# Kernel tuning notes

Measured on AMD Instinct MI355X. Metric: run time of the kernel, lower is better.

## Reference

```python
import jax, jax.numpy as jnp
import numpy as np

N = 203769
E = 234355
IN, HID, OUT = 165, 128, 64
EPS = 1e-5


def setup_inputs() -> dict:
    key = jax.random.key(0)
    ks = jax.random.split(key, 12)
    x = jax.random.normal(ks[0], (N, IN), dtype=jnp.float32)
    edge_index = jax.random.randint(ks[1], (2, E), 0, N, dtype=jnp.int64)
    s = lambda fan: 1.0 / np.sqrt(fan)
    W1 = jax.random.uniform(ks[2], (IN, HID), jnp.float32, -s(IN), s(IN))
    b1 = jnp.zeros((HID,), jnp.float32)
    g1 = jnp.ones((HID,), jnp.float32)
    be1 = jnp.zeros((HID,), jnp.float32)
    W2 = jax.random.uniform(ks[3], (HID, OUT), jnp.float32, -s(HID), s(HID))
    b2 = jnp.zeros((OUT,), jnp.float32)
    g2 = jnp.ones((OUT,), jnp.float32)
    be2 = jnp.zeros((OUT,), jnp.float32)
    Wp1 = jax.random.uniform(ks[4], (OUT, OUT), jnp.float32, -s(OUT), s(OUT))
    bp1 = jax.random.uniform(ks[5], (OUT,), jnp.float32, -s(OUT), s(OUT))
    Wp2 = jax.random.uniform(ks[6], (OUT, OUT), jnp.float32, -s(OUT), s(OUT))
    bp2 = jax.random.uniform(ks[7], (OUT,), jnp.float32, -s(OUT), s(OUT))
    return {"x": x, "edge_index": edge_index, "W1": W1, "b1": b1, "g1": g1, "be1": be1,
            "W2": W2, "b2": b2, "g2": g2, "be2": be2,
            "Wp1": Wp1, "bp1": bp1, "Wp2": Wp2, "bp2": bp2}


def gcn_conv(x, W, b, src, dst, n):
    # PyG GCNConv: h = xW; add self-loops; sym-normalized aggregation; + bias
    h = x @ W  # [N, F]
    loop = jnp.arange(n, dtype=src.dtype)
    s = jnp.concatenate([src, loop])
    d = jnp.concatenate([dst, loop])
    w = jnp.ones(s.shape[0], x.dtype)  # edge_weight=None -> ones
    deg = jax.ops.segment_sum(w, d, num_segments=n)
    dinv = jnp.where(deg > 0, jax.lax.rsqrt(deg), 0.0)
    norm = dinv[s] * w * dinv[d]  # [E+N]
    msg = h[s] * norm[:, None]    # gather + scale
    return jax.ops.segment_sum(msg, d, num_segments=n) + b


def batch_norm(x, g, be):
    m = jnp.mean(x, axis=0)
    v = jnp.mean(jnp.square(x - m), axis=0)  # biased var (torch BN)
    return (x - m) * jax.lax.rsqrt(v + EPS) * g + be


def reference(x, edge_index, W1, b1, g1, be1, W2, b2, g2, be2, Wp1, bp1, Wp2, bp2):
    src, dst = edge_index[0], edge_index[1]
    n = x.shape[0]
    h = gcn_conv(x, W1, b1, src, dst, n)
    h = jax.nn.relu(batch_norm(h, g1, be1))  # dropout omitted (eval / deterministic)
    h = gcn_conv(h, W2, b2, src, dst, n)
    h = batch_norm(h, g2, be2)  # last layer: no relu/dropout
    z = jax.nn.relu(h @ Wp1 + bp1) @ Wp2 + bp2
    return (h, z)
```

## Files before the change

kernel.cpp:

```cpp
#include <hip/hip_runtime.h>
#include <hip/hip_bf16.h>

#define N_NODES 203769
#define N_EDGES 234355
#define F_IN    165
#define F_HID   128
#define F_OUT   64
#define BN_EPS  1e-5f
#define NB_SCAN 796
#define KP      192
#define NBLK    1024
#define GB128C  1593
#define RGP     (GB128C * 8)

typedef short bf16x8 __attribute__((ext_vector_type(8)));
typedef unsigned short u16x8 __attribute__((ext_vector_type(8)));
typedef float f32x4 __attribute__((ext_vector_type(4)));

__device__ __forceinline__ unsigned short f2bf(float f) {
    unsigned int u = __builtin_bit_cast(unsigned int, f);
    u += 0x7fffu + ((u >> 16) & 1u);
    return (unsigned short)(u >> 16);
}

__global__ void k_count(const int* __restrict__ dst, int* __restrict__ cnt) {
    int e = blockIdx.x * 256 + threadIdx.x;
    if (e < N_EDGES) atomicAdd(&cnt[dst[e]], 1);
}

__global__ __launch_bounds__(256) void k_scanA(const int* __restrict__ cnt,
                                               int* __restrict__ partials) {
    __shared__ int sm[256];
    int t = threadIdx.x;
    int i = blockIdx.x * 256 + t;
    int v = (i < N_NODES) ? cnt[i] : 0;
    sm[t] = v;
    __syncthreads();
    for (int off = 128; off > 0; off >>= 1) {
        if (t < off) sm[t] += sm[t + off];
        __syncthreads();
    }
    if (t == 0) partials[blockIdx.x] = sm[0];
}

__global__ __launch_bounds__(1024) void k_scanB(int* __restrict__ partials,
                                                int* __restrict__ row_ptr) {
    __shared__ int sm[1024];
    int t = threadIdx.x;
    int v = (t < NB_SCAN) ? partials[t] : 0;
    sm[t] = v;
    __syncthreads();
    for (int off = 1; off < 1024; off <<= 1) {
        int add = (t >= off) ? sm[t - off] : 0;
        __syncthreads();
        sm[t] += add;
        __syncthreads();
    }
    if (t < NB_SCAN) partials[t] = sm[t] - v;
    if (t == NB_SCAN - 1) row_ptr[N_NODES] = sm[t];
}

__global__ __launch_bounds__(256) void k_scanC(const int* __restrict__ cnt,
                                               const int* __restrict__ partials,
                                               int* __restrict__ row_ptr,
                                               int* __restrict__ cursor,
                                               float* __restrict__ dinv) {
    __shared__ int sm[256];
    int t = threadIdx.x;
    int i = blockIdx.x * 256 + t;
    int v = (i < N_NODES) ? cnt[i] : 0;
    sm[t] = v;
    __syncthreads();
    for (int off = 1; off < 256; off <<= 1) {
        int add = (t >= off) ? sm[t - off] : 0;
        __syncthreads();
        sm[t] += add;
        __syncthreads();
    }
    if (i < N_NODES) {
        int p = partials[blockIdx.x] + sm[t] - v;
        row_ptr[i] = p;
        cursor[i] = p;
        dinv[i] = rsqrtf(1.0f + (float)v);
    }
}

__global__ void k_scatter(const int* __restrict__ src, const int* __restrict__ dst,
                          int* __restrict__ cursor, int* __restrict__ csr_src) {
    int e = blockIdx.x * 256 + threadIdx.x;
    if (e < N_EDGES) {
        int pos = atomicAdd(&cursor[dst[e]], 1);
        csr_src[pos] = src[e];
    }
}

__global__ void k_cvt_w(const float* __restrict__ W1, unsigned short* __restrict__ wb) {
    int i = blockIdx.x * 256 + threadIdx.x;
    if (i < F_HID * KP) {
        int n = i / KP, k = i - n * KP;
        float v = (k < F_IN) ? W1[k * F_HID + n] : 0.0f;
        int ng = n >> 4, l16 = n & 15, kb = k >> 5, quad = (k >> 3) & 3, j = k & 7;
        wb[((((size_t)ng * 6 + kb) * 4 + quad) * 16 + l16) * 8 + j] = f2bf(v);
    }
}

__global__ __launch_bounds__(256) void k_cvt_x(const float* __restrict__ x,
                                               unsigned short* __restrict__ xa) {
    __shared__ unsigned short xt[16 * 200];
    const int rg = blockIdx.x;
    const int t = threadIdx.x;
    const int row0 = rg * 16;

    if (row0 + 16 <= N_NODES) {
        const float* slab = x + (size_t)row0 * F_IN;
        for (int u = t; u < 660; u += 256) {
            float4 v = *(const float4*)&slab[u * 4];
            float vv[4] = {v.x, v.y, v.z, v.w};
            int f0 = u * 4;
#pragma unroll
            for (int j = 0; j < 4; j++) {
                int f = f0 + j;
                int r = f / 165;
                int k = f - r * 165;
                xt[r * 200 + k] = f2bf(vv[j]);
            }
        }
    } else {
        for (int u = t; u < 660; u += 256) {
            int f0 = u * 4;
#pragma unroll
            for (int j = 0; j < 4; j++) {
                int f = f0 + j;
                int r = f / 165;
                int k = f - r * 165;
                int row = row0 + r;
                float val = (row < N_NODES) ? x[(size_t)row * F_IN + k] : 0.0f;
                xt[r * 200 + k] = f2bf(val);
            }
        }
    }
    __syncthreads();

    for (int v = t; v < 384; v += 256) {
        int l16 = v & 15;
        int quad = (v >> 4) & 3;
        int kb = v >> 6;
        int k0 = kb * 32 + quad * 8;
        u16x8 uv;
#pragma unroll
        for (int j = 0; j < 8; j++) {
            int k = k0 + j;
            uv[j] = (k < F_IN) ? xt[l16 * 200 + k] : (unsigned short)0;
        }
        *(u16x8*)&xa[((size_t)rg * 384 + v) * 8] = uv;
    }
}

__global__ __launch_bounds__(256) void k_mfma1(const unsigned short* __restrict__ xa,
                                               const unsigned short* __restrict__ wb,
                                               const float* __restrict__ dinv,
                                               float* __restrict__ h1s) {
    const int t = threadIdx.x;
    const int wv = t >> 6;
    const int lane = t & 63;
    const int l16 = lane & 15;
    const int quad = lane >> 4;
    const int rg0 = blockIdx.x * 8 + wv * 2;
    const int lq = quad * 16 + l16;

    f32x4 acc[2][8];
#pragma unroll
    for (int mt = 0; mt < 2; mt++)
#pragma unroll
        for (int nt = 0; nt < 8; nt++)
            acc[mt][nt] = (f32x4){0.0f, 0.0f, 0.0f, 0.0f};

#pragma unroll
    for (int kb = 0; kb < 6; kb++) {
        bf16x8 a[2], b[8];
#pragma unroll
        for (int mt = 0; mt < 2; mt++)
            a[mt] = *(const bf16x8*)&xa[(((size_t)(rg0 + mt) * 6 + kb) * 64 + lq) * 8];
#pragma unroll
        for (int nt = 0; nt < 8; nt++)
            b[nt] = *(const bf16x8*)&wb[(((size_t)nt * 6 + kb) * 64 + lq) * 8];
#pragma unroll
        for (int mt = 0; mt < 2; mt++)
#pragma unroll
            for (int nt = 0; nt < 8; nt++)
                acc[mt][nt] = __builtin_amdgcn_mfma_f32_16x16x32_bf16(
                    a[mt], b[nt], acc[mt][nt], 0, 0, 0);
    }

#pragma unroll
    for (int mt = 0; mt < 2; mt++) {
#pragma unroll
        for (int rgi = 0; rgi < 4; rgi++) {
            int grow = (rg0 + mt) * 16 + quad * 4 + rgi;
            if (grow < N_NODES) {
                float dv = dinv[grow];
                float* orow = h1s + (size_t)grow * F_HID + l16;
#pragma unroll
                for (int nt = 0; nt < 8; nt++)
                    orow[nt * 16] = acc[mt][nt][rgi] * dv;
            }
        }
    }
}

template <int C, int TPN, int NPB>
__global__ __launch_bounds__(256) void k_aggr(const float* __restrict__ hs,
                                              const int* __restrict__ row_ptr,
                                              const int* __restrict__ csr_src,
                                              const float* __restrict__ dinv,
                                              float* __restrict__ out,
                                              float* __restrict__ psum,
                                              float* __restrict__ psq) {
    const int t = threadIdx.x;
    const int q = t & (TPN - 1);
    const int slot = t / TPN;
    float s0 = 0, s1 = 0, s2 = 0, s3 = 0;
    float q0 = 0, q1 = 0, q2 = 0, q3 = 0;

    for (int node = blockIdx.x * NPB + slot; node < N_NODES;
         node += gridDim.x * NPB) {
        int beg = row_ptr[node];
        int end = row_ptr[node + 1];
        float4 acc = *(const float4*)&hs[(size_t)node * C + q * 4];
        for (int e = beg; e < end; e++) {
            int s = csr_src[e];
            float4 v = *(const float4*)&hs[(size_t)s * C + q * 4];
            acc.x += v.x; acc.y += v.y; acc.z += v.z; acc.w += v.w;
        }
        float dv = dinv[node];
        acc.x *= dv; acc.y *= dv; acc.z *= dv; acc.w *= dv;
        *(float4*)&out[(size_t)node * C + q * 4] = acc;
        s0 += acc.x; s1 += acc.y; s2 += acc.z; s3 += acc.w;
        q0 = fmaf(acc.x, acc.x, q0); q1 = fmaf(acc.y, acc.y, q1);
        q2 = fmaf(acc.z, acc.z, q2); q3 = fmaf(acc.w, acc.w, q3);
    }

    __shared__ float sm[256 * 4];
    __shared__ float sq[256 * 4];
    sm[t * 4 + 0] = s0; sm[t * 4 + 1] = s1; sm[t * 4 + 2] = s2; sm[t * 4 + 3] = s3;
    sq[t * 4 + 0] = q0; sq[t * 4 + 1] = q1; sq[t * 4 + 2] = q2; sq[t * 4 + 3] = q3;
    __syncthreads();
    if (t < TPN) {
#pragma unroll
        for (int sl = 1; sl < NPB; sl++) {
            int u = (sl * TPN + t) * 4;
            s0 += sm[u + 0]; s1 += sm[u + 1]; s2 += sm[u + 2]; s3 += sm[u + 3];
            q0 += sq[u + 0]; q1 += sq[u + 1]; q2 += sq[u + 2]; q3 += sq[u + 3];
        }
        float4 o1 = {s0, s1, s2, s3};
        float4 o2 = {q0, q1, q2, q3};
        *(float4*)&psum[(size_t)blockIdx.x * C + t * 4] = o1;
        *(float4*)&psq [(size_t)blockIdx.x * C + t * 4] = o2;
    }
}

template <int C>
__global__ __launch_bounds__(1024) void k_bn_fin(const float* __restrict__ psum,
                                                 const float* __restrict__ psq,
                                                 const float* __restrict__ g,
                                                 const float* __restrict__ be,
                                                 float* __restrict__ sc,
                                                 float* __restrict__ sh) {
    const int t = threadIdx.x;
    const int c = t & (C - 1);
    const int gg = t / C;
    const int G = 1024 / C;
    const int BPG = NBLK / G;
    float s = 0.0f, sq_ = 0.0f;
    for (int i = 0; i < BPG; i++) {
        int b = gg * BPG + i;
        s   += psum[(size_t)b * C + c];
        sq_ += psq [(size_t)b * C + c];
    }
    __shared__ float sm[1024];
    __shared__ float s2[1024];
    sm[t] = s;
    s2[t] = sq_;
    __syncthreads();
    for (int off = G / 2; off > 0; off >>= 1) {
        if (gg < off) {
            sm[t] += sm[t + off * C];
            s2[t] += s2[t + off * C];
        }
        __syncthreads();
    }
    if (gg == 0) {
        const float invn = 1.0f / (float)N_NODES;
        float mean = sm[c] * invn;
        float var = s2[c] * invn - mean * mean;
        float rstd = rsqrtf(var + BN_EPS);
        float scale = g[c] * rstd;
        sc[c] = scale;
        sh[c] = fmaf(-mean, scale, be[c]);
    }
}

__global__ __launch_bounds__(256) void k_gemm2(const float* __restrict__ out1,
                                               const float* __restrict__ sc1,
                                               const float* __restrict__ sh1,
                                               const float* __restrict__ W2,
                                               const float* __restrict__ dinv,
                                               float* __restrict__ h2s) {
    __shared__ float xs[64 * 132];
    const int row0 = blockIdx.x * 64;
    const int t = threadIdx.x;
    {
        const float* src = out1 + (size_t)row0 * F_HID;
        const int maxe = (N_NODES - row0) * F_HID;
        for (int fi = t; fi < 64 * F_HID; fi += 256) {
            int r = fi >> 7;
            int c = fi & 127;
            float v = (fi < maxe) ? src[fi] : 0.0f;
            v = fmaf(v, sc1[c], sh1[c]);
            xs[r * 132 + c] = fmaxf(v, 0.0f);
        }
    }
    __syncthreads();

    const int c0 = (t & 15) * 4;
    const int r0 = (t >> 4) * 4;

    float acc[4][4];
#pragma unroll
    for (int r = 0; r < 4; r++)
#pragma unroll
        for (int c = 0; c < 4; c++) acc[r][c] = 0.0f;

#pragma unroll 2
    for (int k4 = 0; k4 < F_HID; k4 += 4) {
        float4 xv[4];
#pragma unroll
        for (int r = 0; r < 4; r++)
            xv[r] = *(const float4*)&xs[(r0 + r) * 132 + k4];
        float4 w[4];
#pragma unroll
        for (int j = 0; j < 4; j++)
            w[j] = *(const float4*)&W2[(k4 + j) * F_OUT + c0];
#pragma unroll
        for (int r = 0; r < 4; r++) {
            const float xr[4] = {xv[r].x, xv[r].y, xv[r].z, xv[r].w};
#pragma unroll
            for (int j = 0; j < 4; j++) {
                acc[r][0] = fmaf(xr[j], w[j].x, acc[r][0]);
                acc[r][1] = fmaf(xr[j], w[j].y, acc[r][1]);
                acc[r][2] = fmaf(xr[j], w[j].z, acc[r][2]);
                acc[r][3] = fmaf(xr[j], w[j].w, acc[r][3]);
            }
        }
    }
#pragma unroll
    for (int r = 0; r < 4; r++) {
        int row = row0 + r0 + r;
        if (row < N_NODES) {
            float dv = dinv[row];
            float4 o = {acc[r][0] * dv, acc[r][1] * dv, acc[r][2] * dv, acc[r][3] * dv};
            *(float4*)&h2s[(size_t)row * F_OUT + c0] = o;
        }
    }
}

__global__ __launch_bounds__(256) void k_final(const float* __restrict__ out2,
                                               const float* __restrict__ sc2,
                                               const float* __restrict__ sh2,
                                               const float* __restrict__ Wp1,
                                               const float* __restrict__ bp1,
                                               const float* __restrict__ Wp2,
                                               const float* __restrict__ bp2,
                                               float* __restrict__ out) {
    __shared__ float hs[64 * 68];
    __shared__ float as_[64 * 68];
    const int row0 = blockIdx.x * 64;
    const int t = threadIdx.x;

    {
        const float4* src = (const float4*)out2;
        float4* dsth = (float4*)out;
#pragma unroll
        for (int i = 0; i < 4; i++) {
            int f4 = t + i * 256;
            int r = f4 >> 4;
            int c4 = f4 & 15;
            int grow = row0 + r;
            float4 v = {0, 0, 0, 0};
            if (grow < N_NODES) v = src[(size_t)grow * 16 + c4];
            int c = c4 * 4;
            v.x = fmaf(v.x, sc2[c + 0], sh2[c + 0]);
            v.y = fmaf(v.y, sc2[c + 1], sh2[c + 1]);
            v.z = fmaf(v.z, sc2[c + 2], sh2[c + 2]);
            v.w = fmaf(v.w, sc2[c + 3], sh2[c + 3]);
            if (grow < N_NODES) dsth[(size_t)grow * 16 + c4] = v;
            *(float4*)&hs[r * 68 + c] = v;
        }
    }
    __syncthreads();

    const int c0 = (t & 15) * 4;
    const int r0 = (t >> 4) * 4;

    {
        float acc[4][4];
#pragma unroll
        for (int r = 0; r < 4; r++)
#pragma unroll
            for (int c = 0; c < 4; c++) acc[r][c] = 0.0f;
#pragma unroll 2
        for (int k4 = 0; k4 < 64; k4 += 4) {
            float4 xv[4];
#pragma unroll
            for (int r = 0; r < 4; r++)
                xv[r] = *(const float4*)&hs[(r0 + r) * 68 + k4];
            float4 w[4];
#pragma unroll
            for (int j = 0; j < 4; j++)
                w[j] = *(const float4*)&Wp1[(k4 + j) * 64 + c0];
#pragma unroll
            for (int r = 0; r < 4; r++) {
                const float xr[4] = {xv[r].x, xv[r].y, xv[r].z, xv[r].w};
#pragma unroll
                for (int j = 0; j < 4; j++) {
                    acc[r][0] = fmaf(xr[j], w[j].x, acc[r][0]);
                    acc[r][1] = fmaf(xr[j], w[j].y, acc[r][1]);
                    acc[r][2] = fmaf(xr[j], w[j].z, acc[r][2]);
                    acc[r][3] = fmaf(xr[j], w[j].w, acc[r][3]);
                }
            }
        }
        float4 b = *(const float4*)&bp1[c0];
#pragma unroll
        for (int r = 0; r < 4; r++) {
            float4 o = {fmaxf(acc[r][0] + b.x, 0.0f), fmaxf(acc[r][1] + b.y, 0.0f),
                        fmaxf(acc[r][2] + b.z, 0.0f), fmaxf(acc[r][3] + b.w, 0.0f)};
            *(float4*)&as_[(r0 + r) * 68 + c0] = o;
        }
    }
    __syncthreads();

    {
        float acc[4][4];
#pragma unroll
        for (int r = 0; r < 4; r++)
#pragma unroll
            for (int c = 0; c < 4; c++) acc[r][c] = 0.0f;
#pragma unroll 2
        for (int k4 = 0; k4 < 64; k4 += 4) {
            float4 xv[4];
#pragma unroll
            for (int r = 0; r < 4; r++)
                xv[r] = *(const float4*)&as_[(r0 + r) * 68 + k4];
            float4 w[4];
#pragma unroll
            for (int j = 0; j < 4; j++)
                w[j] = *(const float4*)&Wp2[(k4 + j) * 64 + c0];
#pragma unroll
            for (int r = 0; r < 4; r++) {
                const float xr[4] = {xv[r].x, xv[r].y, xv[r].z, xv[r].w};
#pragma unroll
                for (int j = 0; j < 4; j++) {
                    acc[r][0] = fmaf(xr[j], w[j].x, acc[r][0]);
                    acc[r][1] = fmaf(xr[j], w[j].y, acc[r][1]);
                    acc[r][2] = fmaf(xr[j], w[j].z, acc[r][2]);
                    acc[r][3] = fmaf(xr[j], w[j].w, acc[r][3]);
                }
            }
        }
        float4 b = *(const float4*)&bp2[c0];
        float* zout = out + (size_t)N_NODES * 64;
#pragma unroll
        for (int r = 0; r < 4; r++) {
            int row = row0 + r0 + r;
            if (row < N_NODES) {
                float4 o = {acc[r][0] + b.x, acc[r][1] + b.y,
                            acc[r][2] + b.z, acc[r][3] + b.w};
                *(float4*)&zout[(size_t)row * 64 + c0] = o;
            }
        }
    }
}

extern "C" void kernel_launch(void* const* d_in, const int* in_sizes, int n_in,
                              void* d_out, int out_size, void* d_ws, size_t ws_size,
                              hipStream_t stream) {
    const float* x   = (const float*)d_in[0];
    const int*   ei  = (const int*)d_in[1];
    const float* W1  = (const float*)d_in[2];
    const float* g1  = (const float*)d_in[4];
    const float* be1 = (const float*)d_in[5];
    const float* W2  = (const float*)d_in[6];
    const float* g2  = (const float*)d_in[8];
    const float* be2 = (const float*)d_in[9];
    const float* Wp1 = (const float*)d_in[10];
    const float* bp1 = (const float*)d_in[11];
    const float* Wp2 = (const float*)d_in[12];
    const float* bp2 = (const float*)d_in[13];

    const int* src = ei;
    const int* dst = ei + N_EDGES;

    float* ws = (float*)d_ws;
    float* A    = ws;
    float* B    = A + (size_t)N_NODES * 128;
    float* dinv = B + (size_t)N_NODES * 128;
    float* st   = dinv + N_NODES;
    float* sc1  = st + 256;  float* sh1  = st + 384;
    float* sc2  = st + 640;  float* sh2  = st + 704;
    int* cnt      = (int*)(st + 768);
    int* row_ptr  = cnt + N_NODES;
    int* cursor   = row_ptr + N_NODES + 1;
    int* csr_src  = cursor + N_NODES;
    int* partials = csr_src + N_EDGES;
    unsigned short* wb = (unsigned short*)(partials + NB_SCAN);

    size_t off = (size_t)((char*)(wb + F_HID * KP) - (char*)d_ws);
    off = (off + 15) & ~(size_t)15;
    float* ps1  = (float*)((char*)d_ws + off);
    float* ps1q = ps1 + (size_t)NBLK * 128;
    float* ps2  = ps1q + (size_t)NBLK * 128;
    float* ps2q = ps2 + (size_t)NBLK * 64;
    unsigned short* xa = (unsigned short*)(ps2q + (size_t)NBLK * 64);

    hipMemsetAsync(st, 0, (768 + N_NODES) * sizeof(float), stream);

    const int EB = (N_EDGES + 255) / 256;
    const int GB64 = (N_NODES + 63) / 64;

    k_count<<<EB, 256, 0, stream>>>(dst, cnt);
    k_cvt_w<<<(F_HID * KP + 255) / 256, 256, 0, stream>>>(W1, wb);
    k_cvt_x<<<RGP, 256, 0, stream>>>(x, xa);
    k_scanA<<<NB_SCAN, 256, 0, stream>>>(cnt, partials);
    k_scanB<<<1, 1024, 0, stream>>>(partials, row_ptr);
    k_scanC<<<NB_SCAN, 256, 0, stream>>>(cnt, partials, row_ptr, cursor, dinv);
    k_scatter<<<EB, 256, 0, stream>>>(src, dst, cursor, csr_src);

    k_mfma1<<<GB128C, 256, 0, stream>>>(xa, wb, dinv, A);
    k_aggr<128, 32, 8><<<NBLK, 256, 0, stream>>>(A, row_ptr, csr_src, dinv, B, ps1, ps1q);
    k_bn_fin<128><<<1, 1024, 0, stream>>>(ps1, ps1q, g1, be1, sc1, sh1);

    k_gemm2<<<GB64, 256, 0, stream>>>(B, sc1, sh1, W2, dinv, A);
    k_aggr<64, 16, 16><<<NBLK, 256, 0, stream>>>(A, row_ptr, csr_src, dinv, B, ps2, ps2q);
    k_bn_fin<64><<<1, 1024, 0, stream>>>(ps2, ps2q, g2, be2, sc2, sh2);

    k_final<<<GB64, 256, 0, stream>>>(B, sc2, sh2, Wp1, bp1, Wp2, bp2, (float*)d_out);
}
```

Before: 601.5 us.

## Replace FP32 layer-2 GEMM with split-bf16 MFMA kernel

Replaces the scalar FP32 shared-memory GEMM for layer 2 with an MFMA kernel. Activations (after BN+ReLU) and W2 are each split into bf16 high and low parts, and three MFMAs per tile (hi*hi, lo*hi, hi*lo) keep near-FP32 accuracy. W2 is pre-split by a new small conversion kernel into an MFMA-friendly layout. The aim is to cut VALU FMA cost and the LDS staging, in exchange for extra conversion arithmetic and a slightly different rounding behaviour.

Measured after the change: 546.7 us. -9.1%, faster.

```diff
diff --git a/kernel.cpp b/kernel.cpp
--- a/kernel.cpp
+++ b/kernel.cpp
@@ -22,6 +22,10 @@
     u += 0x7fffu + ((u >> 16) & 1u);
     return (unsigned short)(u >> 16);
 }
+__device__ __forceinline__ float bf2f(unsigned short h) {
+    unsigned int u = ((unsigned int)h) << 16;
+    return __builtin_bit_cast(float, u);
+}
 
 __global__ void k_count(const int* __restrict__ dst, int* __restrict__ cnt) {
     int e = blockIdx.x * 256 + threadIdx.x;
@@ -101,6 +105,22 @@
         float v = (k < F_IN) ? W1[k * F_HID + n] : 0.0f;
         int ng = n >> 4, l16 = n & 15, kb = k >> 5, quad = (k >> 3) & 3, j = k & 7;
         wb[((((size_t)ng * 6 + kb) * 4 + quad) * 16 + l16) * 8 + j] = f2bf(v);
+    }
+}
+
+__global__ void k_cvt_w2(const float* __restrict__ W2,
+                         unsigned short* __restrict__ w2h,
+                         unsigned short* __restrict__ w2l) {
+    int i = blockIdx.x * 256 + threadIdx.x;
+    if (i < F_HID * F_OUT) {
+        int k = i / F_OUT, n = i - k * F_OUT;
+        float v = W2[i];
+        unsigned short h = f2bf(v);
+        float lo = v - bf2f(h);
+        int ng = n >> 4, l16 = n & 15, kb = k >> 5, quad = (k >> 3) & 3, j = k & 7;
+        size_t idx = ((((size_t)ng * 4 + kb) * 4 + quad) * 16 + l16) * 8 + j;
+        w2h[idx] = h;
+        w2l[idx] = f2bf(lo);
     }
 }
 
@@ -202,6 +222,102 @@
                 float* orow = h1s + (size_t)grow * F_HID + l16;
 #pragma unroll
                 for (int nt = 0; nt < 8; nt++)
+                    orow[nt * 16] = acc[mt][nt][rgi] * dv;
+            }
+        }
+    }
+}
+
+__global__ __launch_bounds__(256) void k_mfma2(const float* __restrict__ out1,
+                                               const float* __restrict__ sc1,
+                                               const float* __restrict__ sh1,
+                                               const unsigned short* __restrict__ w2h,
+                                               const unsigned short* __restrict__ w2l,
+                                               const float* __restrict__ dinv,
+                                               float* __restrict__ h2s) {
+    const int t = threadIdx.x;
+    const int wv = t >> 6;
+    const int lane = t & 63;
+    const int l16 = lane & 15;
+    const int quad = lane >> 4;
+    const int rg0 = blockIdx.x * 8 + wv * 2;
+    const int lq = quad * 16 + l16;
+
+    f32x4 acc[2][4];
+#pragma unroll
+    for (int mt = 0; mt < 2; mt++)
+#pragma unroll
+        for (int nt = 0; nt < 4; nt++)
+            acc[mt][nt] = (f32x4){0.0f, 0.0f, 0.0f, 0.0f};
+
+#pragma unroll
+    for (int kb = 0; kb < 4; kb++) {
+        const int k0 = kb * 32 + quad * 8;
+        float4 sA = *(const float4*)&sc1[k0];
+        float4 sB = *(const float4*)&sc1[k0 + 4];
+        float4 hA = *(const float4*)&sh1[k0];
+        float4 hB = *(const float4*)&sh1[k0 + 4];
+        float sv[8] = {sA.x, sA.y, sA.z, sA.w, sB.x, sB.y, sB.z, sB.w};
+        float hv[8] = {hA.x, hA.y, hA.z, hA.w, hB.x, hB.y, hB.z, hB.w};
+
+        bf16x8 bh[4], bl[4];
+#pragma unroll
+        for (int nt = 0; nt < 4; nt++) {
+            size_t u = ((((size_t)nt * 4 + kb) * 64) + lq) * 8;
+            bh[nt] = *(const bf16x8*)&w2h[u];
+            bl[nt] = *(const bf16x8*)&w2l[u];
+        }
+
+        bf16x8 ah[2], al[2];
+#pragma unroll
+        for (int mt = 0; mt < 2; mt++) {
+            int row = (rg0 + mt) * 16 + l16;
+            float v[8];
+            if (row < N_NODES) {
+                const float* rp = out1 + (size_t)row * F_HID + k0;
+                float4 v0 = *(const float4*)rp;
+                float4 v1 = *(const float4*)(rp + 4);
+                v[0] = v0.x; v[1] = v0.y; v[2] = v0.z; v[3] = v0.w;
+                v[4] = v1.x; v[5] = v1.y; v[6] = v1.z; v[7] = v1.w;
+            } else {
+#pragma unroll
+                for (int j = 0; j < 8; j++) v[j] = 0.0f;
+            }
+            u16x8 uh, ul;
+#pragma unroll
+            for (int j = 0; j < 8; j++) {
+                float f = fmaxf(fmaf(v[j], sv[j], hv[j]), 0.0f);
+                unsigned short hb = f2bf(f);
+                uh[j] = hb;
+                ul[j] = f2bf(f - bf2f(hb));
+            }
+            ah[mt] = __builtin_bit_cast(bf16x8, uh);
+            al[mt] = __builtin_bit_cast(bf16x8, ul);
+        }
+
+#pragma unroll
+        for (int mt = 0; mt < 2; mt++)
+#pragma unroll
+            for (int nt = 0; nt < 4; nt++) {
+                acc[mt][nt] = __builtin_amdgcn_mfma_f32_16x16x32_bf16(
+                    ah[mt], bh[nt], acc[mt][nt], 0, 0, 0);
+                acc[mt][nt] = __builtin_amdgcn_mfma_f32_16x16x32_bf16(
+                    al[mt], bh[nt], acc[mt][nt], 0, 0, 0);
+                acc[mt][nt] = __builtin_amdgcn_mfma_f32_16x16x32_bf16(
+                    ah[mt], bl[nt], acc[mt][nt], 0, 0, 0);
+            }
+    }
+
+#pragma unroll
+    for (int mt = 0; mt < 2; mt++) {
+#pragma unroll
+        for (int rgi = 0; rgi < 4; rgi++) {
+            int grow = (rg0 + mt) * 16 + quad * 4 + rgi;
+            if (grow < N_NODES) {
+                float dv = dinv[grow];
+                float* orow = h2s + (size_t)grow * F_OUT + l16;
+#pragma unroll
+                for (int nt = 0; nt < 4; nt++)
                     orow[nt * 16] = acc[mt][nt][rgi] * dv;
             }
         }
@@ -300,70 +416,6 @@
     }
 }
 
-__global__ __launch_bounds__(256) void k_gemm2(const float* __restrict__ out1,
-                                               const float* __restrict__ sc1,
-                                               const float* __restrict__ sh1,
-                                               const float* __restrict__ W2,
-                                               const float* __restrict__ dinv,
-                                               float* __restrict__ h2s) {
-    __shared__ float xs[64 * 132];
-    const int row0 = blockIdx.x * 64;
-    const int t = threadIdx.x;
-    {
-        const float* src = out1 + (size_t)row0 * F_HID;
-        const int maxe = (N_NODES - row0) * F_HID;
-        for (int fi = t; fi < 64 * F_HID; fi += 256) {
-            int r = fi >> 7;
-            int c = fi & 127;
-            float v = (fi < maxe) ? src[fi] : 0.0f;
-            v = fmaf(v, sc1[c], sh1[c]);
-            xs[r * 132 + c] = fmaxf(v, 0.0f);
-        }
-    }
-    __syncthreads();
-
-    const int c0 = (t & 15) * 4;
-    const int r0 = (t >> 4) * 4;
-
-    float acc[4][4];
-#pragma unroll
-    for (int r = 0; r < 4; r++)
-#pragma unroll
-        for (int c = 0; c < 4; c++) acc[r][c] = 0.0f;
-
-#pragma unroll 2
-    for (int k4 = 0; k4 < F_HID; k4 += 4) {
-        float4 xv[4];
-#pragma unroll
-        for (int r = 0; r < 4; r++)
-            xv[r] = *(const float4*)&xs[(r0 + r) * 132 + k4];
-        float4 w[4];
-#pragma unroll
-        for (int j = 0; j < 4; j++)
-            w[j] = *(const float4*)&W2[(k4 + j) * F_OUT + c0];
-#pragma unroll
-        for (int r = 0; r < 4; r++) {
-            const float xr[4] = {xv[r].x, xv[r].y, xv[r].z, xv[r].w};
-#pragma unroll
-            for (int j = 0; j < 4; j++) {
-                acc[r][0] = fmaf(xr[j], w[j].x, acc[r][0]);
-                acc[r][1] = fmaf(xr[j], w[j].y, acc[r][1]);
-                acc[r][2] = fmaf(xr[j], w[j].z, acc[r][2]);
-                acc[r][3] = fmaf(xr[j], w[j].w, acc[r][3]);
-            }
-        }
-    }
-#pragma unroll
-    for (int r = 0; r < 4; r++) {
-        int row = row0 + r0 + r;
-        if (row < N_NODES) {
-            float dv = dinv[row];
-            float4 o = {acc[r][0] * dv, acc[r][1] * dv, acc[r][2] * dv, acc[r][3] * dv};
-            *(float4*)&h2s[(size_t)row * F_OUT + c0] = o;
-        }
-    }
-}
-
 __global__ __launch_bounds__(256) void k_final(const float* __restrict__ out2,
                                                const float* __restrict__ sc2,
                                                const float* __restrict__ sh2,
@@ -514,8 +566,10 @@
     int* csr_src  = cursor + N_NODES;
     int* partials = csr_src + N_EDGES;
     unsigned short* wb = (unsigned short*)(partials + NB_SCAN);
-
-    size_t off = (size_t)((char*)(wb + F_HID * KP) - (char*)d_ws);
+    unsigned short* w2h = wb + (size_t)F_HID * KP;
+    unsigned short* w2l = w2h + (size_t)F_HID * F_OUT;
+
+    size_t off = (size_t)((char*)(w2l + F_HID * F_OUT) - (char*)d_ws);
     off = (off + 15) & ~(size_t)15;
     float* ps1  = (float*)((char*)d_ws + off);
     float* ps1q = ps1 + (size_t)NBLK * 128;
@@ -530,6 +584,7 @@
 
     k_count<<<EB, 256, 0, stream>>>(dst, cnt);
     k_cvt_w<<<(F_HID * KP + 255) / 256, 256, 0, stream>>>(W1, wb);
+    k_cvt_w2<<<(F_HID * F_OUT + 255) / 256, 256, 0, stream>>>(W2, w2h, w2l);
     k_cvt_x<<<RGP, 256, 0, stream>>>(x, xa);
     k_scanA<<<NB_SCAN, 256, 0, stream>>>(cnt, partials);
     k_scanB<<<1, 1024, 0, stream>>>(partials, row_ptr);
@@ -540,7 +595,7 @@
     k_aggr<128, 32, 8><<<NBLK, 256, 0, stream>>>(A, row_ptr, csr_src, dinv, B, ps1, ps1q);
     k_bn_fin<128><<<1, 1024, 0, stream>>>(ps1, ps1q, g1, be1, sc1, sh1);
 
-    k_gemm2<<<GB64, 256, 0, stream>>>(B, sc1, sh1, W2, dinv, A);
+    k_mfma2<<<GB128C, 256, 0, stream>>>(B, sc1, sh1, w2h, w2l, dinv, A);
     k_aggr<64, 16, 16><<<NBLK, 256, 0, stream>>>(A, row_ptr, csr_src, dinv, B, ps2, ps2q);
     k_bn_fin<64><<<1, 1024, 0, stream>>>(ps2, ps2q, g2, be2, sc2, sh2);
 
```
